# Kernel tuning notes

Measured on AMD Instinct MI355X. Metric: run time of the kernel, lower is better.

Reference implementation:

```python
import jax, jax.numpy as jnp
import numpy as np
import math

EMBED_DIM = 128
NUM_HEADS = 8
HDIM = EMBED_DIM // NUM_HEADS


def setup_inputs() -> dict:
    key = jax.random.key(0)
    kq, kh, km, k1, k2, k3, k4 = jax.random.split(key, 7)
    B, NQ, GS = 32, 1024, 1024
    q = jax.random.normal(kq, (B, NQ, EMBED_DIM), dtype=jnp.float32)
    h = jax.random.normal(kh, (B, GS, EMBED_DIM), dtype=jnp.float32)
    mask = jax.random.bernoulli(km, 0.15, (B, NQ, GS))
    stdv = 1.0 / math.sqrt(HDIM)
    Wq = jax.random.uniform(k1, (NUM_HEADS, EMBED_DIM, HDIM), jnp.float32, -stdv, stdv)
    Wk = jax.random.uniform(k2, (NUM_HEADS, EMBED_DIM, HDIM), jnp.float32, -stdv, stdv)
    Wv = jax.random.uniform(k3, (NUM_HEADS, EMBED_DIM, HDIM), jnp.float32, -stdv, stdv)
    stdv_o = 1.0 / math.sqrt(EMBED_DIM)
    Wout = jax.random.uniform(k4, (NUM_HEADS, HDIM, EMBED_DIM), jnp.float32, -stdv_o, stdv_o)
    return {"q": q, "h": h, "mask": mask, "Wq": Wq, "Wk": Wk, "Wv": Wv, "Wout": Wout}


def reference(q, h, mask, Wq, Wk, Wv, Wout):
    norm = 1.0 / math.sqrt(HDIM)
    # per-head projections: [h, b, n, e]
    Q = jnp.einsum('bnd,hde->hbne', q, Wq)
    K = jnp.einsum('bgd,hde->hbge', h, Wk)
    V = jnp.einsum('bgd,hde->hbge', h, Wv)
    compat = norm * jnp.einsum('hbne,hbge->hbng', Q, K)  # [h,b,nq,gs]
    m = mask[None]  # broadcast over heads
    compat = jnp.where(m, -jnp.inf, compat)
    attn = jax.nn.softmax(compat, axis=-1)
    attn = jnp.where(m, 0.0, attn)
    heads = jnp.einsum('hbng,hbge->hbne', attn, V)
    out = jnp.einsum('hbne,hed->bnd', heads, Wout)
    return out
```

## Files before the change

kernel.cpp:

```cpp
#include <hip/hip_runtime.h>

typedef unsigned short u16;
typedef unsigned int   u32;
typedef short bf16x8 __attribute__((ext_vector_type(8)));
typedef float f32x4  __attribute__((ext_vector_type(4)));

#define NB  32
#define NQ  1024
#define GS  1024
#define NH  8
#define SCQ (0.25f * 1.4426950408889634f)
#define MBIG (-1.0e30f)

#define MFMA16(a, b, c) __builtin_amdgcn_mfma_f32_16x16x32_bf16(a, b, c, 0, 0, 0)

__device__ __forceinline__ u16 f2bf(float f) {
    u32 u = __float_as_uint(f);
    return (u16)((u + 0x7fffu + ((u >> 16) & 1u)) >> 16);
}
__device__ __forceinline__ u32 pk2bf(float a, float b) {
    u32 ua = (__float_as_uint(a) + 0x8000u) >> 16;
    u32 ub = (__float_as_uint(b) + 0x8000u) & 0xffff0000u;
    return ua | ub;
}
__device__ __forceinline__ u32 packbf2(float a, float b) {
#if __has_builtin(__builtin_amdgcn_cvt_pk_bf16_f32)
    auto pk = __builtin_amdgcn_cvt_pk_bf16_f32(a, b);
    u32 w;
    __builtin_memcpy(&w, &pk, 4);
    return w;
#else
    return pk2bf(a, b);
#endif
}

template <int MODE>
__device__ __forceinline__ void mgemm(const float* __restrict__ Ain,
                                      const float* __restrict__ Wsrc,
                                      float wscale,
                                      u16* __restrict__ outb,
                                      u16* As, u16* Ws, int row0) {
    const int t    = threadIdx.x;
    const int wv   = t >> 6;
    const int lane = t & 63;
    const int quad = lane >> 4;
    const int c    = lane & 15;

#pragma unroll
    for (int g0 = 0; g0 < 2048; g0 += 256) {
        int g = g0 + t;
        int row = g >> 4, k0 = (g & 15) * 8;
        const float4* ap = (const float4*)&Ain[(size_t)(row0 + row) * 128 + k0];
        float4 a0 = ap[0], a1 = ap[1];
        int4 pk;
        pk.x = (int)pk2bf(a0.x, a0.y);
        pk.y = (int)pk2bf(a0.z, a0.w);
        pk.z = (int)pk2bf(a1.x, a1.y);
        pk.w = (int)pk2bf(a1.z, a1.w);
        *(int4*)&As[row * 136 + k0] = pk;
    }
#pragma unroll
    for (int i0 = 0; i0 < 16384; i0 += 256) {
        int i = i0 + t;
        float v = Wsrc[i];
        int hh = i >> 11, d = (i >> 4) & 127, e = i & 15;
        Ws[(hh * 16 + e) * 136 + d] = f2bf(v * wscale);
    }
    __syncthreads();

    const f32x4 zf = {0.f, 0.f, 0.f, 0.f};
    f32x4 acc[2][8];
#pragma unroll
    for (int s = 0; s < 2; ++s)
#pragma unroll
        for (int j = 0; j < 8; ++j) acc[s][j] = zf;

#pragma unroll
    for (int kt = 0; kt < 4; ++kt) {
        bf16x8 af0 = *(const bf16x8*)&As[(wv * 32 + c) * 136 + kt * 32 + quad * 8];
        bf16x8 af1 = *(const bf16x8*)&As[(wv * 32 + 16 + c) * 136 + kt * 32 + quad * 8];
#pragma unroll
        for (int j = 0; j < 8; ++j) {
            bf16x8 bfr = *(const bf16x8*)&Ws[(j * 16 + c) * 136 + kt * 32 + quad * 8];
            acc[0][j] = MFMA16(af0, bfr, acc[0][j]);
            acc[1][j] = MFMA16(af1, bfr, acc[1][j]);
        }
    }

#pragma unroll
    for (int s = 0; s < 2; ++s)
#pragma unroll
        for (int j = 0; j < 8; ++j)
#pragma unroll
            for (int r = 0; r < 4; ++r) {
                int row = row0 + wv * 32 + s * 16 + quad * 4 + r;
                int col = j * 16 + c;
                float v = acc[s][j][r];
                if (MODE == 0) {
                    outb[(size_t)row * 128 + col] = f2bf(v);
                } else {
                    int bI = row >> 10, tb = row & 1023;
                    outb[(size_t)bI * (128 * 1024) + (size_t)col * 1024 + tb] = f2bf(v);
                }
            }
}

__global__ __launch_bounds__(256, 2) void proj_mfma(const float* __restrict__ q,
                                                    const float* __restrict__ h,
                                                    const float* __restrict__ Wq,
                                                    const float* __restrict__ Wk,
                                                    const float* __restrict__ Wv,
                                                    const float* __restrict__ Wout,
                                                    u16* __restrict__ Qb,
                                                    u16* __restrict__ Kb,
                                                    u16* __restrict__ Vtg,
                                                    u16* __restrict__ Wob) {
    __shared__ u16 As[128 * 136];
    __shared__ u16 Ws[128 * 136];
    int row0 = blockIdx.x * 128;
    if (blockIdx.y == 0 && blockIdx.x == 0) {
        for (int i = threadIdx.x; i < 16384; i += 256) {
            int d = i >> 7, k = i & 127, hh = k >> 4, e = k & 15;
            Wob[i] = f2bf(Wout[hh * 2048 + e * 128 + d]);
        }
    }
    if (blockIdx.y == 0)      mgemm<0>(q, Wq, SCQ,  Qb,  As, Ws, row0);
    else if (blockIdx.y == 1) mgemm<0>(h, Wk, 1.0f, Kb,  As, Ws, row0);
    else                      mgemm<2>(h, Wv, 1.0f, Vtg, As, Ws, row0);
}

__global__ __launch_bounds__(512, 4) void flash_mfma(const u16* __restrict__ Qb,
                                                     const u16* __restrict__ Kb,
                                                     const u16* __restrict__ Vtg,
                                                     const int* __restrict__ mask,
                                                     const u16* __restrict__ Wob,
                                                     float* __restrict__ out) {
    __shared__ u16 Kt[32 * 136];
    __shared__ u16 Vtt[128 * 36];
    __shared__ u16 Ps[NH][32 * 36];
    __shared__ float Mf[32 * 36];

    const int b    = blockIdx.x;
    const int q0   = blockIdx.y * 32;
    const int t    = threadIdx.x;
    const int hh   = t >> 6;
    const int lane = t & 63;
    const int quad = lane >> 4;
    const int c    = lane & 15;

    const f32x4  zf = {0.f, 0.f, 0.f, 0.f};
    const bf16x8 zb = {0, 0, 0, 0, 0, 0, 0, 0};

    bf16x8 qf[2];
#pragma unroll
    for (int s = 0; s < 2; ++s) {
        qf[s] = zb;
        if (quad < 2)
            qf[s] = *(const bf16x8*)&Qb[((size_t)b * NQ + q0 + s * 16 + c) * 128 +
                                        hh * 16 + quad * 8];
    }

    f32x4 O[2] = {zf, zf};
    float ls[2][4] = {{0.f, 0.f, 0.f, 0.f}, {0.f, 0.f, 0.f, 0.f}};

    const int skey = t >> 4;
    const int sd0  = (t & 15) * 8;
    const int vdim = t >> 2;
    const int vq   = t & 3;
    const int mrow = t >> 4;
    const int mk0  = (t & 15) * 2;

    const u16* Kbase = &Kb[((size_t)b * GS + skey) * 128 + sd0];
    const u16* Vbase = &Vtg[(size_t)b * (128 * 1024) + (size_t)vdim * 1024];
    const int* Mbase = &mask[((size_t)b * NQ + q0 + mrow) * GS + mk0];

    int4 kreg = *(const int4*)Kbase;
    int2 va   = *(const int2*)(Vbase + vq * 4);
    int2 vb   = *(const int2*)(Vbase + 16 + vq * 4);
    int2 mreg = *(const int2*)Mbase;

    for (int g0 = 0; g0 < GS; g0 += 32) {
        __syncthreads();
        *(int4*)&Kt[skey * 136 + sd0] = kreg;
        {
            int4 w;
            w.x = (int)(((u32)va.x & 0xffffu) | ((u32)vb.x << 16));
            w.y = (int)(((u32)va.x >> 16) | ((u32)vb.x & 0xffff0000u));
            w.z = (int)(((u32)va.y & 0xffffu) | ((u32)vb.y << 16));
            w.w = (int)(((u32)va.y >> 16) | ((u32)vb.y & 0xffff0000u));
            *(int4*)&Vtt[vdim * 36 + vq * 8] = w;
        }
        Mf[mk0 * 36 + mrow]       = mreg.x ? MBIG : 0.f;
        Mf[(mk0 + 1) * 36 + mrow] = mreg.y ? MBIG : 0.f;
        __syncthreads();

        if (g0 + 32 < GS) {
            kreg = *(const int4*)(Kbase + (size_t)(g0 + 32) * 128);
            va   = *(const int2*)(Vbase + g0 + 32 + vq * 4);
            vb   = *(const int2*)(Vbase + g0 + 48 + vq * 4);
            mreg = *(const int2*)(Mbase + (g0 + 32));
        }

        f32x4 sc[2][2];
#pragma unroll
        for (int kt = 0; kt < 2; ++kt) {
            bf16x8 kf = zb;
            if (quad < 2)
                kf = *(const bf16x8*)&Kt[(kt * 16 + c) * 136 + hh * 16 + quad * 8];
#pragma unroll
            for (int s = 0; s < 2; ++s) {
                f32x4 c0 = *(const f32x4*)&Mf[(kt * 16 + c) * 36 + s * 16 + quad * 4];
                sc[s][kt] = MFMA16(qf[s], kf, c0);
            }
        }
        bf16x8 vf = *(const bf16x8*)&Vtt[(hh * 16 + c) * 36 + quad * 8];

#pragma unroll
        for (int s = 0; s < 2; ++s) {
#pragma unroll
            for (int r = 0; r < 4; ++r) {
                float e0 = exp2f(sc[s][0][r]);
                float e1 = exp2f(sc[s][1][r]);
                ls[s][r] += e0 + e1;
                int row = s * 16 + quad * 4 + r;
                *(u32*)&Ps[hh][row * 36 + 2 * c] = packbf2(e0, e1);
            }
        }

#pragma unroll
        for (int s = 0; s < 2; ++s) {
            bf16x8 pf = *(const bf16x8*)&Ps[hh][(s * 16 + c) * 36 + quad * 8];
            O[s] = MFMA16(pf, vf, O[s]);
        }
    }

    float rl[2][4];
#pragma unroll
    for (int s = 0; s < 2; ++s)
#pragma unroll
        for (int r = 0; r < 4; ++r) {
            float l = ls[s][r];
            l += __shfl_xor(l, 1);
            l += __shfl_xor(l, 2);
            l += __shfl_xor(l, 4);
            l += __shfl_xor(l, 8);
            rl[s][r] = (l > 0.f) ? 1.f / l : 0.f;
        }
    __syncthreads();
    u16* Hs = Kt;
#pragma unroll
    for (int s = 0; s < 2; ++s)
#pragma unroll
        for (int r = 0; r < 4; ++r)
            Hs[(s * 16 + quad * 4 + r) * 136 + hh * 16 + c] = f2bf(O[s][r] * rl[s][r]);
    __syncthreads();

    f32x4 oacc[2] = {zf, zf};
#pragma unroll
    for (int kt = 0; kt < 4; ++kt) {
        bf16x8 bfr = *(const bf16x8*)&Wob[(hh * 16 + c) * 128 + kt * 32 + quad * 8];
#pragma unroll
        for (int s = 0; s < 2; ++s) {
            bf16x8 af = *(const bf16x8*)&Hs[(s * 16 + c) * 136 + kt * 32 + quad * 8];
            oacc[s] = MFMA16(af, bfr, oacc[s]);
        }
    }
#pragma unroll
    for (int s = 0; s < 2; ++s)
#pragma unroll
        for (int r = 0; r < 4; ++r)
            out[((size_t)b * NQ + q0 + s * 16 + quad * 4 + r) * 128 + hh * 16 + c] =
                oacc[s][r];
}

extern "C" void kernel_launch(void* const* d_in, const int* in_sizes, int n_in,
                              void* d_out, int out_size, void* d_ws, size_t ws_size,
                              hipStream_t stream) {
    const float* q    = (const float*)d_in[0];
    const float* h    = (const float*)d_in[1];
    const int*   mask = (const int*)d_in[2];
    const float* Wq   = (const float*)d_in[3];
    const float* Wk   = (const float*)d_in[4];
    const float* Wv   = (const float*)d_in[5];
    const float* Wout = (const float*)d_in[6];
    float* out = (float*)d_out;

    const size_t NTOK = (size_t)NB * NQ;
    u16* Qb  = (u16*)d_ws;
    u16* Kb  = Qb + NTOK * 128;
    u16* Vtg = Kb + NTOK * 128;
    u16* Wob = Vtg + NTOK * 128;

    proj_mfma<<<dim3(256, 3), 256, 0, stream>>>(q, h, Wq, Wk, Wv, Wout,
                                                Qb, Kb, Vtg, Wob);
    flash_mfma<<<dim3(NB, NQ / 32), 512, 0, stream>>>(Qb, Kb, Vtg, mask, Wob, out);
}
```

Measured before the change: 322.8 us.

## Pretranspose weights in a prep kernel and permute mask LDS layout

Adds a small wprep kernel that converts Wq/Wk/Wv/Wout to bf16 once, already transposed and scaled, so each projection block does a plain vectorized int4 copy into shared memory. Before, every block did a scattered scalar transpose-convert of the weights. The mask tile in shared memory is written with a permuted row index, and the MFMA accumulator-init load uses a matching offset, to change the LDS bank access pattern. The P pack also switches from the hardware cvt_pk builtin to a manual rounding pack. In exchange it adds one extra kernel launch.

```diff
diff --git a/kernel.cpp b/kernel.cpp
--- a/kernel.cpp
+++ b/kernel.cpp
@@ -23,21 +23,27 @@
     u32 ub = (__float_as_uint(b) + 0x8000u) & 0xffff0000u;
     return ua | ub;
 }
-__device__ __forceinline__ u32 packbf2(float a, float b) {
-#if __has_builtin(__builtin_amdgcn_cvt_pk_bf16_f32)
-    auto pk = __builtin_amdgcn_cvt_pk_bf16_f32(a, b);
-    u32 w;
-    __builtin_memcpy(&w, &pk, 4);
-    return w;
-#else
-    return pk2bf(a, b);
-#endif
+
+__global__ __launch_bounds__(256) void wprep(const float* __restrict__ Wq,
+                                             const float* __restrict__ Wk,
+                                             const float* __restrict__ Wv,
+                                             const float* __restrict__ Wout,
+                                             u16* __restrict__ Wp) {
+    int m  = blockIdx.x >> 3;
+    int sl = blockIdx.x & 7;
+    const float* src = (m == 0) ? Wq : (m == 1) ? Wk : (m == 2) ? Wv : Wout;
+    float sc = (m == 0) ? SCQ : 1.0f;
+    for (int i = sl * 2048 + threadIdx.x; i < (sl + 1) * 2048; i += 256) {
+        float v;
+        if (m < 3) { int cc = i >> 7, k = i & 127;  v = src[(cc >> 4) * 2048 + k * 16 + (cc & 15)]; }
+        else       { int d  = i >> 7, he = i & 127; v = src[(he >> 4) * 2048 + (he & 15) * 128 + d]; }
+        Wp[m * 16384 + i] = f2bf(v * sc);
+    }
 }
 
 template <int MODE>
 __device__ __forceinline__ void mgemm(const float* __restrict__ Ain,
-                                      const float* __restrict__ Wsrc,
-                                      float wscale,
+                                      const u16* __restrict__ Wpm,
                                       u16* __restrict__ outb,
                                       u16* As, u16* Ws, int row0) {
     const int t    = threadIdx.x;
@@ -60,11 +66,10 @@
         *(int4*)&As[row * 136 + k0] = pk;
     }
 #pragma unroll
-    for (int i0 = 0; i0 < 16384; i0 += 256) {
-        int i = i0 + t;
-        float v = Wsrc[i];
-        int hh = i >> 11, d = (i >> 4) & 127, e = i & 15;
-        Ws[(hh * 16 + e) * 136 + d] = f2bf(v * wscale);
+    for (int g0 = 0; g0 < 2048; g0 += 256) {
+        int g = g0 + t;
+        int cc = g >> 4, k0 = (g & 15) * 8;
+        *(int4*)&Ws[cc * 136 + k0] = *(const int4*)&Wpm[cc * 128 + k0];
     }
     __syncthreads();
 
@@ -107,26 +112,16 @@
 
 __global__ __launch_bounds__(256, 2) void proj_mfma(const float* __restrict__ q,
                                                     const float* __restrict__ h,
-                                                    const float* __restrict__ Wq,
-                                                    const float* __restrict__ Wk,
-                                                    const float* __restrict__ Wv,
-                                                    const float* __restrict__ Wout,
+                                                    const u16* __restrict__ Wp,
                                                     u16* __restrict__ Qb,
                                                     u16* __restrict__ Kb,
-                                                    u16* __restrict__ Vtg,
-                                                    u16* __restrict__ Wob) {
+                                                    u16* __restrict__ Vtg) {
     __shared__ u16 As[128 * 136];
     __shared__ u16 Ws[128 * 136];
     int row0 = blockIdx.x * 128;
-    if (blockIdx.y == 0 && blockIdx.x == 0) {
-        for (int i = threadIdx.x; i < 16384; i += 256) {
-            int d = i >> 7, k = i & 127, hh = k >> 4, e = k & 15;
-            Wob[i] = f2bf(Wout[hh * 2048 + e * 128 + d]);
-        }
-    }
-    if (blockIdx.y == 0)      mgemm<0>(q, Wq, SCQ,  Qb,  As, Ws, row0);
-    else if (blockIdx.y == 1) mgemm<0>(h, Wk, 1.0f, Kb,  As, Ws, row0);
-    else                      mgemm<2>(h, Wv, 1.0f, Vtg, As, Ws, row0);
+    if (blockIdx.y == 0)      mgemm<0>(q, Wp,         Qb,  As, Ws, row0);
+    else if (blockIdx.y == 1) mgemm<0>(h, Wp + 16384, Kb,  As, Ws, row0);
+    else                      mgemm<2>(h, Wp + 32768, Vtg, As, Ws, row0);
 }
 
 __global__ __launch_bounds__(512, 4) void flash_mfma(const u16* __restrict__ Qb,
@@ -169,6 +164,8 @@
     const int vq   = t & 3;
     const int mrow = t >> 4;
     const int mk0  = (t & 15) * 2;
+    const int rp = (mrow & 3) | (((mrow >> 4) & 1) << 2) |
+                   (((mrow >> 3) & 1) << 3) | (((mrow >> 2) & 1) << 4);
 
     const u16* Kbase = &Kb[((size_t)b * GS + skey) * 128 + sd0];
     const u16* Vbase = &Vtg[(size_t)b * (128 * 1024) + (size_t)vdim * 1024];
@@ -178,6 +175,8 @@
     int2 va   = *(const int2*)(Vbase + vq * 4);
     int2 vb   = *(const int2*)(Vbase + 16 + vq * 4);
     int2 mreg = *(const int2*)Mbase;
+
+    const int mfoff = ((quad >> 1) << 3) | ((quad & 1) << 4);
 
     for (int g0 = 0; g0 < GS; g0 += 32) {
         __syncthreads();
@@ -190,8 +189,8 @@
             w.w = (int)(((u32)va.y >> 16) | ((u32)vb.y & 0xffff0000u));
             *(int4*)&Vtt[vdim * 36 + vq * 8] = w;
         }
-        Mf[mk0 * 36 + mrow]       = mreg.x ? MBIG : 0.f;
-        Mf[(mk0 + 1) * 36 + mrow] = mreg.y ? MBIG : 0.f;
+        Mf[mk0 * 36 + rp]       = mreg.x ? MBIG : 0.f;
+        Mf[(mk0 + 1) * 36 + rp] = mreg.y ? MBIG : 0.f;
         __syncthreads();
 
         if (g0 + 32 < GS) {
@@ -209,7 +208,7 @@
                 kf = *(const bf16x8*)&Kt[(kt * 16 + c) * 136 + hh * 16 + quad * 8];
 #pragma unroll
             for (int s = 0; s < 2; ++s) {
-                f32x4 c0 = *(const f32x4*)&Mf[(kt * 16 + c) * 36 + s * 16 + quad * 4];
+                f32x4 c0 = *(const f32x4*)&Mf[(kt * 16 + c) * 36 + (s << 2) + mfoff];
                 sc[s][kt] = MFMA16(qf[s], kf, c0);
             }
         }
@@ -223,7 +222,7 @@
                 float e1 = exp2f(sc[s][1][r]);
                 ls[s][r] += e0 + e1;
                 int row = s * 16 + quad * 4 + r;
-                *(u32*)&Ps[hh][row * 36 + 2 * c] = packbf2(e0, e1);
+                *(u32*)&Ps[hh][row * 36 + 2 * c] = pk2bf(e0, e1);
             }
         }
 
@@ -289,9 +288,10 @@
     u16* Qb  = (u16*)d_ws;
     u16* Kb  = Qb + NTOK * 128;
     u16* Vtg = Kb + NTOK * 128;
-    u16* Wob = Vtg + NTOK * 128;
-
-    proj_mfma<<<dim3(256, 3), 256, 0, stream>>>(q, h, Wq, Wk, Wv, Wout,
-                                                Qb, Kb, Vtg, Wob);
-    flash_mfma<<<dim3(NB, NQ / 32), 512, 0, stream>>>(Qb, Kb, Vtg, mask, Wob, out);
-}
+    u16* Wp  = Vtg + NTOK * 128;
+
+    wprep<<<dim3(32), 256, 0, stream>>>(Wq, Wk, Wv, Wout, Wp);
+    proj_mfma<<<dim3(256, 3), 256, 0, stream>>>(q, h, Wp, Qb, Kb, Vtg);
+    flash_mfma<<<dim3(NB, NQ / 32), 512, 0, stream>>>(Qb, Kb, Vtg, mask,
+                                                      Wp + 49152, out);
+}
```

Result: no change. 316.6 us (-1.9%).
